# Kernel tuning notes

Measured on AMD Instinct MI355X. Metric: run time of the kernel, lower is better.

## Reference

```python
import jax, jax.numpy as jnp
from jax import lax
import numpy as np

P = 1        # padding width
REF0 = 2     # reference rows/cols (ref[0]) -> conv input channels
WP = 3       # window width (ref[1]) -> conv kernel size along border
HID = 8      # hidden channels


def _make_branch(key):
    k = jax.random.split(key, 6)
    s1 = 1.0 / np.sqrt(REF0 * WP)
    s2 = 1.0 / np.sqrt(HID)
    w1 = jax.random.uniform(k[0], (HID, REF0, WP, 1), jnp.float32, -s1, s1)
    b1 = jax.random.uniform(k[1], (HID,), jnp.float32, -s1, s1)
    w2 = jax.random.uniform(k[2], (HID, HID), jnp.float32, -s2, s2)
    b2 = jax.random.uniform(k[3], (HID,), jnp.float32, -s2, s2)
    w3 = jax.random.uniform(k[4], (1, HID), jnp.float32, -s2, s2)
    b3 = jax.random.uniform(k[5], (1,), jnp.float32, -s2, s2)
    return w1, b1, w2, b2, w3, b3


def setup_inputs() -> dict:
    key = jax.random.key(0)
    ks = jax.random.split(key, 5)
    x = jax.random.normal(ks[0], (32, 64, 224, 224), jnp.float32)
    d = {"x": x}
    for j, n in enumerate(["t", "b", "l", "r"]):
        w1, b1, w2, b2, w3, b3 = _make_branch(ks[j + 1])
        d[f"{n}w1"], d[f"{n}b1"] = w1, b1
        d[f"{n}w2"], d[f"{n}b2"] = w2, b2
        d[f"{n}w3"], d[f"{n}b3"] = w3, b3
    return d


def _mlp(s, w1, b1, w2, b2, w3, b3):
    # s: [B, REF0, L, C]  (border rows as channels, spatial = (border length, feature channels))
    y = lax.conv_general_dilated(s, w1, (1, 1), "VALID",
                                 dimension_numbers=("NCHW", "OIHW", "NCHW"))
    y = jax.nn.relu(y + b1[None, :, None, None])          # [B, HID, L-2, C]
    y = jax.nn.relu(jnp.einsum("bhlc,oh->bolc", y, w2) + b2[None, :, None, None])
    y = jax.nn.relu(jnp.einsum("bhlc,oh->bolc", y, w3) + b3[None, :, None, None])
    return y[:, 0]                                        # [B, L-2, C]


def reference(x,
              tw1, tb1, tw2, tb2, tw3, tb3,
              bw1, bb1, bw2, bb2, bw3, bb3,
              lw1, lb1, lw2, lb2, lw3, lb3,
              rw1, rb1, rw2, rb2, rw3, rb3):
    B, C, H, W = x.shape
    p = P
    H2, W2 = H + 2 * p, W + 2 * p
    xp = jnp.zeros((B, C, H2, W2), x.dtype).at[:, :, p:H + p, p:W + p].set(x)
    for i in range(p):  # sequential ring updates (data-dependent recurrence)
        top = jnp.transpose(xp[:, :, p - i:p + REF0 - i, :], (0, 2, 3, 1))  # [B,REF0,W2,C]
        xp = xp.at[:, :, p - 1 - i, 1:W2 - 1].set(
            jnp.transpose(_mlp(top, tw1, tb1, tw2, tb2, tw3, tb3), (0, 2, 1)))
        bot = jnp.transpose(xp[:, :, p + H - REF0 + i:p + H + i, :], (0, 2, 3, 1))
        xp = xp.at[:, :, p + H + i, 1:W2 - 1].set(
            jnp.transpose(_mlp(bot, bw1, bb1, bw2, bb2, bw3, bb3), (0, 2, 1)))
        left = jnp.transpose(xp[:, :, :, p - i:p + REF0 - i], (0, 3, 2, 1))  # [B,REF0,H2,C]
        xp = xp.at[:, :, 1:H2 - 1, p - 1 - i].set(
            jnp.transpose(_mlp(left, lw1, lb1, lw2, lb2, lw3, lb3), (0, 2, 1)))
        right = jnp.transpose(xp[:, :, :, p + W - REF0 + i:p + W + i], (0, 3, 2, 1))
        xp = xp.at[:, :, 1:H2 - 1, p + W + i].set(
            jnp.transpose(_mlp(right, rw1, rb1, rw2, rb2, rw3, rb3), (0, 2, 1)))
    return xp
```

## Files before the change

### kernel.cpp

```cpp
#include <hip/hip_runtime.h>

#define BB   32
#define CC   64
#define HH   224
#define WW   224
#define H2   226
#define W2   226
#define HID  8

constexpr unsigned NPLANE   = BB * CC;
constexpr unsigned XHW      = HH * WW;
constexpr unsigned HW2      = H2 * W2;
constexpr unsigned F4PLANE  = HW2 / 4;
constexpr unsigned GPP      = 50;
constexpr unsigned NBORD    = NPLANE * HH;
constexpr size_t   NXTOT    = (size_t)NPLANE * XHW;

__global__ __launch_bounds__(256) void pad_copy_k(const float* __restrict__ x,
                                                  float* __restrict__ out) {
    __shared__ __align__(16) float lds[1056];
    const unsigned t  = threadIdx.x;
    const unsigned g  = blockIdx.x;
    const unsigned p  = blockIdx.y;

    const unsigned o0 = g * 1024u;
    const unsigned h0 = o0 / 226u;
    const unsigned w0 = o0 - 226u * h0;
    int L0 = (int)(224u * h0 + w0) - 225 - 3;
    if (L0 < 0) L0 = 0;
    L0 &= ~3;

    const size_t pbase = (size_t)p * XHW;
    for (unsigned i = t; i < 264u; i += 256u) {
        size_t gi = pbase + (unsigned)L0 + 4u * i;
        if (gi > NXTOT - 4u) gi = NXTOT - 4u;
        const float4 v = *reinterpret_cast<const float4*>(x + gi);
        *reinterpret_cast<float4*>(&lds[4u * i]) = v;
    }
    __syncthreads();

    const unsigned f4 = g * 256u + t;
    if (f4 >= F4PLANE) return;
    const unsigned o = o0 + 4u * t;
    const unsigned h = o / 226u;
    const unsigned w = o - 226u * h;
    float vals[4];
#pragma unroll
    for (int e = 0; e < 4; ++e) {
        unsigned we = w + (unsigned)e;
        unsigned he = h;
        if (we >= 226u) { we -= 226u; ++he; }
        const bool inter = ((he - 1u) < (unsigned)HH) & ((we - 1u) < (unsigned)WW);
        const int li = (int)(224u * he + we) - 225 - L0;
        const unsigned lic = inter ? (unsigned)li : 0u;
        const float vv = lds[lic];
        vals[e] = inter ? vv : 0.f;
    }
    reinterpret_cast<float4*>(out + (size_t)p * HW2)[f4] =
        make_float4(vals[0], vals[1], vals[2], vals[3]);
}

__device__ __forceinline__ float mlp_eval(const float s[2][3],
                                          const float* __restrict__ W) {
    const float* W1  = W;
    const float* B1  = W + 48;
    const float* W2m = W + 56;
    const float* B2  = W + 120;
    const float* W3  = W + 128;
    const float  b3  = W[136];
    float y1[HID];
#pragma unroll
    for (int h = 0; h < HID; ++h) {
        float a = B1[h];
#pragma unroll
        for (int r = 0; r < 2; ++r)
#pragma unroll
            for (int k = 0; k < 3; ++k)
                a = fmaf(s[r][k], W1[h * 6 + r * 3 + k], a);
        y1[h] = fmaxf(a, 0.f);
    }
    float y2[HID];
#pragma unroll
    for (int o = 0; o < HID; ++o) {
        float a = B2[o];
#pragma unroll
        for (int h = 0; h < HID; ++h) a = fmaf(y1[h], W2m[o * 8 + h], a);
        y2[o] = fmaxf(a, 0.f);
    }
    float a = b3;
#pragma unroll
    for (int h = 0; h < HID; ++h) a = fmaf(y2[h], W3[h], a);
    return fmaxf(a, 0.f);
}

__device__ __forceinline__ void load_wts(unsigned t, float* W,
                                         const float* w1, const float* b1,
                                         const float* w2, const float* b2,
                                         const float* w3, const float* b3) {
    if (t < 48u) W[t] = w1[t];
    if (t < 64u) W[56u + t] = w2[t];
    if (t < 8u) {
        W[48u + t]  = b1[t];
        W[120u + t] = b2[t];
        W[128u + t] = w3[t];
    }
    if (t == 0u) W[136] = b3[0];
}

__global__ __launch_bounds__(256) void border_tb_k(
    const float* __restrict__ x, float* __restrict__ out,
    const float* tw1, const float* tb1, const float* tw2, const float* tb2,
    const float* tw3, const float* tb3,
    const float* bw1, const float* bb1, const float* bw2, const float* bb2,
    const float* bw3, const float* bb3) {
    const bool top = (blockIdx.y == 0);
    __shared__ float W[137];
    load_wts(threadIdx.x, W,
             top ? tw1 : bw1, top ? tb1 : bb1, top ? tw2 : bw2,
             top ? tb2 : bb2, top ? tw3 : bw3, top ? tb3 : bb3);
    __syncthreads();

    const unsigned gid = blockIdx.x * 256u + threadIdx.x;
    const unsigned l   = gid % (unsigned)HH;
    const unsigned bc  = gid / (unsigned)HH;

    const unsigned r0 = top ? 0u : (unsigned)(HH - 2);
    float s[2][3];
#pragma unroll
    for (int r = 0; r < 2; ++r)
#pragma unroll
        for (int k = 0; k < 3; ++k) {
            unsigned xc = l + (unsigned)k - 1u;
            s[r][k] = (xc < (unsigned)WW)
                          ? x[bc * XHW + (r0 + (unsigned)r) * (unsigned)WW + xc]
                          : 0.f;
        }
    const float res = mlp_eval(s, W);
    const unsigned orow = top ? 0u : (unsigned)(H2 - 1);
    out[bc * HW2 + orow * (unsigned)W2 + (l + 1u)] = res;
}

__global__ __launch_bounds__(256) void border_lr_k(
    const float* __restrict__ x, float* __restrict__ out,
    const float* lw1, const float* lb1, const float* lw2, const float* lb2,
    const float* lw3, const float* lb3,
    const float* rw1, const float* rb1, const float* rw2, const float* rb2,
    const float* rw3, const float* rb3) {
    const bool left = (blockIdx.y == 0);
    __shared__ float W[137];
    load_wts(threadIdx.x, W,
             left ? lw1 : rw1, left ? lb1 : rb1, left ? lw2 : rw2,
             left ? lb2 : rb2, left ? lw3 : rw3, left ? lb3 : rb3);
    __syncthreads();

    const unsigned gid = blockIdx.x * 256u + threadIdx.x;
    const unsigned l   = gid % (unsigned)HH;
    const unsigned bc  = gid / (unsigned)HH;

    const unsigned cc0 = left ? 0u : (unsigned)(WW - 2);
    const unsigned oc0 = left ? 1u : (unsigned)(W2 - 3);
    float s[2][3];
#pragma unroll
    for (int k = 0; k < 3; ++k) {
        const unsigned pr = l + (unsigned)k;
        float v0, v1;
        if (pr == 0u) {
            v0 = out[bc * HW2 + oc0];
            v1 = out[bc * HW2 + oc0 + 1u];
        } else if (pr == (unsigned)(H2 - 1)) {
            v0 = out[bc * HW2 + (unsigned)(H2 - 1) * W2 + oc0];
            v1 = out[bc * HW2 + (unsigned)(H2 - 1) * W2 + oc0 + 1u];
        } else {
            const float2 t2 = *reinterpret_cast<const float2*>(
                x + bc * XHW + (pr - 1u) * (unsigned)WW + cc0);
            v0 = t2.x;
            v1 = t2.y;
        }
        s[0][k] = v0;
        s[1][k] = v1;
    }
    const float res = mlp_eval(s, W);
    out[bc * HW2 + (l + 1u) * (unsigned)W2 + (left ? 0u : (unsigned)(W2 - 1))] = res;
}

extern "C" void kernel_launch(void* const* d_in, const int* in_sizes, int n_in,
                              void* d_out, int out_size, void* d_ws,
                              size_t ws_size, hipStream_t stream) {
    const float* x = (const float*)d_in[0];
    const float* w[24];
    for (int i = 0; i < 24; ++i) w[i] = (const float*)d_in[1 + i];
    float* out = (float*)d_out;

    pad_copy_k<<<dim3(GPP, NPLANE), dim3(256), 0, stream>>>(x, out);

    border_tb_k<<<dim3(NBORD / 256u, 2), dim3(256), 0, stream>>>(
        x, out, w[0], w[1], w[2], w[3], w[4], w[5],
        w[6], w[7], w[8], w[9], w[10], w[11]);

    border_lr_k<<<dim3(NBORD / 256u, 2), dim3(256), 0, stream>>>(
        x, out, w[12], w[13], w[14], w[15], w[16], w[17],
        w[18], w[19], w[20], w[21], w[22], w[23]);
}
```

Baseline: 218.1 us.

## Fuse border kernels by recomputing corner values; use nontemporal stores in pad copy

The top/bottom and left/right border kernels become one launch with four branch families. Left and right threads no longer read the corner values written by the top and bottom pass; they recompute them in place with the top and bottom MLPs, which removes the dependency between the two launches. Separately, the padded-copy kernel now writes its output with nontemporal stores to reduce cache pollution on the large streaming write. The costs are extra redundant MLP work at the corner rows, plus every block loading all four weight sets.

```diff
diff --git a/kernel.cpp b/kernel.cpp
--- a/kernel.cpp
+++ b/kernel.cpp
@@ -15,6 +15,10 @@
 constexpr unsigned GPP      = 50;
 constexpr unsigned NBORD    = NPLANE * HH;
 constexpr size_t   NXTOT    = (size_t)NPLANE * XHW;
+
+typedef float f4 __attribute__((ext_vector_type(4)));
+
+struct WPtrs { const float* p[24]; };
 
 __global__ __launch_bounds__(256) void pad_copy_k(const float* __restrict__ x,
                                                   float* __restrict__ out) {
@@ -34,13 +38,13 @@
     for (unsigned i = t; i < 264u; i += 256u) {
         size_t gi = pbase + (unsigned)L0 + 4u * i;
         if (gi > NXTOT - 4u) gi = NXTOT - 4u;
-        const float4 v = *reinterpret_cast<const float4*>(x + gi);
-        *reinterpret_cast<float4*>(&lds[4u * i]) = v;
+        const f4 v = *reinterpret_cast<const f4*>(x + gi);
+        *reinterpret_cast<f4*>(&lds[4u * i]) = v;
     }
     __syncthreads();
 
-    const unsigned f4 = g * 256u + t;
-    if (f4 >= F4PLANE) return;
+    const unsigned f4i = g * 256u + t;
+    if (f4i >= F4PLANE) return;
     const unsigned o = o0 + 4u * t;
     const unsigned h = o / 226u;
     const unsigned w = o - 226u * h;
@@ -56,8 +60,10 @@
         const float vv = lds[lic];
         vals[e] = inter ? vv : 0.f;
     }
-    reinterpret_cast<float4*>(out + (size_t)p * HW2)[f4] =
-        make_float4(vals[0], vals[1], vals[2], vals[3]);
+    f4 res;
+    res.x = vals[0]; res.y = vals[1]; res.z = vals[2]; res.w = vals[3];
+    __builtin_nontemporal_store(
+        res, reinterpret_cast<f4*>(out + (size_t)p * HW2) + f4i);
 }
 
 __device__ __forceinline__ float mlp_eval(const float s[2][3],
@@ -93,111 +99,89 @@
     return fmaxf(a, 0.f);
 }
 
-__device__ __forceinline__ void load_wts(unsigned t, float* W,
-                                         const float* w1, const float* b1,
-                                         const float* w2, const float* b2,
-                                         const float* w3, const float* b3) {
-    if (t < 48u) W[t] = w1[t];
-    if (t < 64u) W[56u + t] = w2[t];
-    if (t < 8u) {
-        W[48u + t]  = b1[t];
-        W[120u + t] = b2[t];
-        W[128u + t] = w3[t];
-    }
-    if (t == 0u) W[136] = b3[0];
-}
-
-__global__ __launch_bounds__(256) void border_tb_k(
-    const float* __restrict__ x, float* __restrict__ out,
-    const float* tw1, const float* tb1, const float* tw2, const float* tb2,
-    const float* tw3, const float* tb3,
-    const float* bw1, const float* bb1, const float* bw2, const float* bb2,
-    const float* bw3, const float* bb3) {
-    const bool top = (blockIdx.y == 0);
-    __shared__ float W[137];
-    load_wts(threadIdx.x, W,
-             top ? tw1 : bw1, top ? tb1 : bb1, top ? tw2 : bw2,
-             top ? tb2 : bb2, top ? tw3 : bw3, top ? tb3 : bb3);
-    __syncthreads();
-
-    const unsigned gid = blockIdx.x * 256u + threadIdx.x;
-    const unsigned l   = gid % (unsigned)HH;
-    const unsigned bc  = gid / (unsigned)HH;
-
-    const unsigned r0 = top ? 0u : (unsigned)(HH - 2);
+__device__ __forceinline__ float eval_tb(const float* __restrict__ xp,
+                                         const float* __restrict__ W,
+                                         unsigned l, unsigned r0) {
     float s[2][3];
 #pragma unroll
     for (int r = 0; r < 2; ++r)
 #pragma unroll
         for (int k = 0; k < 3; ++k) {
             unsigned xc = l + (unsigned)k - 1u;
-            s[r][k] = (xc < (unsigned)WW)
-                          ? x[bc * XHW + (r0 + (unsigned)r) * (unsigned)WW + xc]
-                          : 0.f;
+            s[r][k] = (xc < (unsigned)WW) ? xp[(r0 + (unsigned)r) * WW + xc] : 0.f;
         }
-    const float res = mlp_eval(s, W);
-    const unsigned orow = top ? 0u : (unsigned)(H2 - 1);
-    out[bc * HW2 + orow * (unsigned)W2 + (l + 1u)] = res;
+    return mlp_eval(s, W);
 }
 
-__global__ __launch_bounds__(256) void border_lr_k(
-    const float* __restrict__ x, float* __restrict__ out,
-    const float* lw1, const float* lb1, const float* lw2, const float* lb2,
-    const float* lw3, const float* lb3,
-    const float* rw1, const float* rb1, const float* rw2, const float* rb2,
-    const float* rw3, const float* rb3) {
-    const bool left = (blockIdx.y == 0);
-    __shared__ float W[137];
-    load_wts(threadIdx.x, W,
-             left ? lw1 : rw1, left ? lb1 : rb1, left ? lw2 : rw2,
-             left ? lb2 : rb2, left ? lw3 : rw3, left ? lb3 : rb3);
+__global__ __launch_bounds__(256) void border_k(const float* __restrict__ x,
+                                                float* __restrict__ out,
+                                                WPtrs wp) {
+    __shared__ float wts[4][137];
+    const unsigned t = threadIdx.x;
+#pragma unroll
+    for (int br = 0; br < 4; ++br) {
+        const float* const* b = wp.p + 6 * br;
+        if (t < 48u) wts[br][t] = b[0][t];
+        if (t < 64u) wts[br][56u + t] = b[2][t];
+        if (t < 8u) {
+            wts[br][48u + t]  = b[1][t];
+            wts[br][120u + t] = b[3][t];
+            wts[br][128u + t] = b[4][t];
+        }
+        if (t == 0u) wts[br][136] = b[5][0];
+    }
     __syncthreads();
 
-    const unsigned gid = blockIdx.x * 256u + threadIdx.x;
+    const unsigned gid = blockIdx.x * 256u + t;
     const unsigned l   = gid % (unsigned)HH;
     const unsigned bc  = gid / (unsigned)HH;
+    const unsigned fam = blockIdx.y;
 
-    const unsigned cc0 = left ? 0u : (unsigned)(WW - 2);
-    const unsigned oc0 = left ? 1u : (unsigned)(W2 - 3);
-    float s[2][3];
+    const float* xp = x + (size_t)bc * XHW;
+    float*       op = out + (size_t)bc * HW2;
+
+    if (fam < 2u) {
+        const bool top = (fam == 0u);
+        const float res = eval_tb(xp, wts[fam], l, top ? 0u : (unsigned)(HH - 2));
+        op[(top ? 0u : (unsigned)(H2 - 1)) * W2 + l + 1u] = res;
+    } else {
+        const bool left    = (fam == 2u);
+        const unsigned cc0 = left ? 0u : (unsigned)(WW - 2);
+        const unsigned oc0 = left ? 1u : (unsigned)(W2 - 3);
+        float s[2][3];
 #pragma unroll
-    for (int k = 0; k < 3; ++k) {
-        const unsigned pr = l + (unsigned)k;
-        float v0, v1;
-        if (pr == 0u) {
-            v0 = out[bc * HW2 + oc0];
-            v1 = out[bc * HW2 + oc0 + 1u];
-        } else if (pr == (unsigned)(H2 - 1)) {
-            v0 = out[bc * HW2 + (unsigned)(H2 - 1) * W2 + oc0];
-            v1 = out[bc * HW2 + (unsigned)(H2 - 1) * W2 + oc0 + 1u];
-        } else {
-            const float2 t2 = *reinterpret_cast<const float2*>(
-                x + bc * XHW + (pr - 1u) * (unsigned)WW + cc0);
-            v0 = t2.x;
-            v1 = t2.y;
+        for (int k = 0; k < 3; ++k) {
+            const unsigned pr = l + (unsigned)k;
+            float v0, v1;
+            if (pr == 0u) {
+                v0 = eval_tb(xp, wts[0], oc0 - 1u, 0u);
+                v1 = eval_tb(xp, wts[0], oc0, 0u);
+            } else if (pr == (unsigned)(H2 - 1)) {
+                v0 = eval_tb(xp, wts[1], oc0 - 1u, (unsigned)(HH - 2));
+                v1 = eval_tb(xp, wts[1], oc0, (unsigned)(HH - 2));
+            } else {
+                const float2 t2 = *reinterpret_cast<const float2*>(
+                    xp + (pr - 1u) * (unsigned)WW + cc0);
+                v0 = t2.x;
+                v1 = t2.y;
+            }
+            s[0][k] = v0;
+            s[1][k] = v1;
         }
-        s[0][k] = v0;
-        s[1][k] = v1;
+        const float res = mlp_eval(s, wts[fam]);
+        op[(l + 1u) * (unsigned)W2 + (left ? 0u : (unsigned)(W2 - 1))] = res;
     }
-    const float res = mlp_eval(s, W);
-    out[bc * HW2 + (l + 1u) * (unsigned)W2 + (left ? 0u : (unsigned)(W2 - 1))] = res;
 }
 
 extern "C" void kernel_launch(void* const* d_in, const int* in_sizes, int n_in,
                               void* d_out, int out_size, void* d_ws,
                               size_t ws_size, hipStream_t stream) {
     const float* x = (const float*)d_in[0];
-    const float* w[24];
-    for (int i = 0; i < 24; ++i) w[i] = (const float*)d_in[1 + i];
+    WPtrs wp;
+    for (int i = 0; i < 24; ++i) wp.p[i] = (const float*)d_in[1 + i];
     float* out = (float*)d_out;
 
     pad_copy_k<<<dim3(GPP, NPLANE), dim3(256), 0, stream>>>(x, out);
 
-    border_tb_k<<<dim3(NBORD / 256u, 2), dim3(256), 0, stream>>>(
-        x, out, w[0], w[1], w[2], w[3], w[4], w[5],
-        w[6], w[7], w[8], w[9], w[10], w[11]);
-
-    border_lr_k<<<dim3(NBORD / 256u, 2), dim3(256), 0, stream>>>(
-        x, out, w[12], w[13], w[14], w[15], w[16], w[17],
-        w[18], w[19], w[20], w[21], w[22], w[23]);
+    border_k<<<dim3(NBORD / 256u, 4), dim3(256), 0, stream>>>(x, out, wp);
 }
```

New measurement: 267.7 us. 1.23x slower.
